# Kernel tuning notes

Measured on AMD Instinct MI355X. Metric: run time of the kernel, lower is better.

The kernel has to match this reference:

```python
import jax, jax.numpy as jnp
import numpy as np

# Regular (dv=3, dc=6) LDPC Tanner graph, rate 1/2
N = 2097152   # variable nodes (code.n)
M = 1048576   # check nodes (H.shape[0])
DV = 3
DC = 6
T = 10        # max_iterations
BC = 4        # c2v bit-width -> 2^(bc-1) = 8 magnitude levels
K = 2 ** (BC - 1)
QUANT_PARAMS = [(2.0, 1.0), (4.0, 1.5), (6.0, 2.0)]


def _make_thresholds():
    """Per-iteration threshold table [T, K]; tau_j = C*(j/(K-1))**gamma."""
    def thr(C, g):
        return [C * (j / (K - 1)) ** g for j in range(K)]
    rows = []
    for t in range(T):
        if t < T // 3:
            C, g = QUANT_PARAMS[0]
        elif t < 2 * T // 3:
            C, g = QUANT_PARAMS[1]
        else:
            C, g = QUANT_PARAMS[-1]
        rows.append(thr(C, g))
    return jnp.asarray(rows, dtype=jnp.float32)


def setup_inputs() -> dict:
    key = jax.random.key(0)
    k_llr, k_beta, k_alpha = jax.random.split(key, 3)
    rng = np.random.default_rng(0)
    # each variable node has exactly DV edges; each check exactly DC edges
    var_idx = np.repeat(np.arange(N, dtype=np.int32), DV)
    chk_idx = rng.permutation(np.repeat(np.arange(M, dtype=np.int32), DC)).astype(np.int32)
    llr = jax.random.normal(k_llr, (N,), dtype=jnp.float32) * 2.0
    # weight init matches nn.Parameter(torch.randn(1)*0.1), one per (iter, degree)
    beta = jax.random.normal(k_beta, (T,), dtype=jnp.float32) * 0.1
    alpha = jax.random.normal(k_alpha, (T,), dtype=jnp.float32) * 0.1
    return {
        "llr": llr,
        "var_idx": jnp.asarray(var_idx),
        "chk_idx": jnp.asarray(chk_idx),
        "beta": beta,
        "alpha": alpha,
        "thresholds": _make_thresholds(),
        "m": M,
    }


def reference(llr, var_idx, chk_idx, beta, alpha, thresholds, m):
    n = llr.shape[0]
    E = var_idx.shape[0]
    eidx = jnp.arange(E, dtype=jnp.int32)
    INF = jnp.float32(jnp.inf)

    def step(v2c, xs):
        b, a, thr = xs  # scalar beta_t, alpha_t, thr [K]
        neg = v2c < 0
        sgn = jnp.where(neg, -1.0, 1.0).astype(v2c.dtype)
        mag = jnp.abs(v2c)
        # --- check node update: min-sum with exclusion (min1/min2) ---
        min1 = jax.ops.segment_min(mag, chk_idx, num_segments=m)
        # first edge attaining the min in each check (ties -> lowest edge id)
        cand = jnp.where(mag <= min1[chk_idx], eidx, E)
        first = jax.ops.segment_min(cand, chk_idx, num_segments=m)
        is_min = eidx == first[chk_idx]
        min2 = jax.ops.segment_min(jnp.where(is_min, INF, mag), chk_idx, num_segments=m)
        min2 = jnp.where(jnp.isinf(min2), min1, min2)  # degree-1 guard
        # sign product excluding self: total parity * own sign
        cnt = jax.ops.segment_sum(neg.astype(jnp.int32), chk_idx, num_segments=m)
        tot = (1 - 2 * (cnt & 1)).astype(v2c.dtype)
        sign_excl = tot[chk_idx] * sgn
        mval = jnp.where(is_min, min2[chk_idx], min1[chk_idx])
        raw = b * sign_excl * mval
        # --- RCQ quantize/dequantize of c2v: snap |raw| down to threshold ---
        q = jnp.clip(jnp.searchsorted(thr, jnp.abs(raw), side="right") - 1, 0, K - 1)
        c2v = jnp.where(raw < 0, -1.0, 1.0) * thr[q]
        # --- variable node update ---
        post = llr + jax.ops.segment_sum(c2v, var_idx, num_segments=n)
        v2c_new = a * (post[var_idx] - c2v)
        return v2c_new, post

    v2c0 = llr[var_idx]
    _, posts = jax.lax.scan(step, v2c0, (beta, alpha, thresholds))
    posterior = posts[-1]
    decoded = (posterior < 0).astype(jnp.int32)
    return decoded, posterior, jnp.int32(beta.shape[0])
```

## Files before the change

### kernel.cpp

```cpp
#include <hip/hip_runtime.h>
#include <stdint.h>

#define NV 2097152
#define MC 1048576
#define EE 6291456
#define TT 10

#define CHUNK 8192
#define NBLK 768
#define FBK 512
#define CPB 2048
#define CSEG 12288
#define FG 512
#define GSEG 12288
#define VBK 256
#define VSEG 24576

__global__ __launch_bounds__(512) void initcur_kernel(uint32_t* __restrict__ gcur) {
    int i = blockIdx.x * 512 + threadIdx.x;
    gcur[i] = (uint32_t)(i & 511) * 12288u;
}

__global__ __launch_bounds__(256) void bin1_kernel(const int* __restrict__ chk_idx,
                                                   uint32_t* __restrict__ gcurA,
                                                   uint32_t* __restrict__ im1_e,
                                                   uint16_t* __restrict__ im1_c) {
    __shared__ uint32_t cnt0[512];
    __shared__ uint32_t aux[512];
    __shared__ uint32_t sA[CHUNK];
    __shared__ uint16_t sB[CHUNK];
    const int tid = threadIdx.x;
    const int rep = tid >> 7;
    const int base = blockIdx.x * CHUNK;
    cnt0[tid] = 0; cnt0[tid + 256] = 0;
    aux[tid] = 0;  aux[tid + 256] = 0;
    __syncthreads();
    int4 cc4[8];
#pragma unroll
    for (int k = 0; k < 8; ++k) cc4[k] = ((const int4*)chk_idx)[(base >> 2) + tid + 256 * k];
    uint32_t br[32];
#pragma unroll
    for (int k = 0; k < 8; ++k) {
        int cv[4] = {cc4[k].x, cc4[k].y, cc4[k].z, cc4[k].w};
#pragma unroll
        for (int ii = 0; ii < 4; ++ii) {
            uint32_t b = (uint32_t)cv[ii] >> 11;
            uint32_t r = atomicAdd(rep ? &aux[b] : &cnt0[b], 1u);
            br[k * 4 + ii] = (b << 13) | r;
        }
    }
    __syncthreads();
    const uint32_t s0 = cnt0[tid] + aux[tid];
    const uint32_t s1 = cnt0[tid + 256] + aux[tid + 256];
    aux[tid] = s0; aux[tid + 256] = s1;
    __syncthreads();
    for (int d = 1; d < 512; d <<= 1) {
        uint32_t a0 = (tid >= d) ? aux[tid - d] : 0u;
        uint32_t a1 = aux[tid + 256 - d];
        __syncthreads();
        aux[tid] += a0; aux[tid + 256] += a1;
        __syncthreads();
    }
    const uint32_t excl0 = aux[tid] - s0;
    const uint32_t excl1 = aux[tid + 256] - s1;
    aux[tid] = excl0; aux[tid + 256] = excl1;
    const uint32_t gb0 = atomicAdd(&gcurA[tid], s0);
    const uint32_t gb1 = atomicAdd(&gcurA[tid + 256], s1);
    __syncthreads();
#pragma unroll
    for (int k = 0; k < 8; ++k) {
        int cv[4] = {cc4[k].x, cc4[k].y, cc4[k].z, cc4[k].w};
#pragma unroll
        for (int ii = 0; ii < 4; ++ii) {
            uint32_t v = br[k * 4 + ii];
            uint32_t b = v >> 13;
            uint32_t r = v & 8191u;
            uint32_t j = aux[b] + (rep ? cnt0[b] : 0u) + r;
            uint32_t e = (uint32_t)(base + (tid + 256 * k) * 4 + ii);
            sA[j] = (b << 23) | e;
            sB[j] = (uint16_t)((uint32_t)cv[ii] & 2047u);
        }
    }
    __syncthreads();
    aux[tid] = gb0 - excl0; aux[tid + 256] = gb1 - excl1;
    __syncthreads();
#pragma unroll 8
    for (int k = 0; k < 32; ++k) {
        int j = tid + 256 * k;
        uint32_t v = sA[j];
        uint32_t b = v >> 23;
        uint32_t addr = aux[b] + (uint32_t)j;
        im1_e[addr] = v & 0x7FFFFFu;
        im1_c[addr] = sB[j];
    }
}

__global__ __launch_bounds__(256) void place1_kernel(const uint32_t* __restrict__ im1_e,
                                                     const uint16_t* __restrict__ im1_c,
                                                     uint32_t* __restrict__ chk_edges,
                                                     uint8_t* __restrict__ b1rank,
                                                     uint32_t* __restrict__ runcntB) {
    __shared__ uint32_t win[CSEG];
    __shared__ uint32_t ccnt[CPB / 2];
    __shared__ uint32_t cntB[VBK];
    const int tid = threadIdx.x, blk = blockIdx.x;
    for (int j = tid; j < CPB / 2; j += 256) ccnt[j] = 0;
    cntB[tid] = 0;
    __syncthreads();
    const size_t cb = (size_t)blk * CSEG;
    for (int k = 0; k < 12; ++k) {
        int j0 = (tid + 256 * k) * 4;
        const uint4 e4 = *(const uint4*)&im1_e[cb + j0];
        const ushort4 c4 = *(const ushort4*)&im1_c[cb + j0];
        uint32_t c, old, s;
        c = c4.x; old = atomicAdd(&ccnt[c >> 1], 1u << ((c & 1) * 16));
        s = (old >> ((c & 1) * 16)) & 0xFFFFu; win[c * 6 + s] = e4.x;
        c = c4.y; old = atomicAdd(&ccnt[c >> 1], 1u << ((c & 1) * 16));
        s = (old >> ((c & 1) * 16)) & 0xFFFFu; win[c * 6 + s] = e4.y;
        c = c4.z; old = atomicAdd(&ccnt[c >> 1], 1u << ((c & 1) * 16));
        s = (old >> ((c & 1) * 16)) & 0xFFFFu; win[c * 6 + s] = e4.z;
        c = c4.w; old = atomicAdd(&ccnt[c >> 1], 1u << ((c & 1) * 16));
        s = (old >> ((c & 1) * 16)) & 0xFFFFu; win[c * 6 + s] = e4.w;
    }
    __syncthreads();
    for (int j = tid; j < CSEG; j += 256) chk_edges[cb + j] = win[j];
    for (int k = 0; k < CSEG / 256; ++k) {
        int lp = tid + 256 * k;
        uint32_t e = win[lp];
        uint32_t bB = (e / 3u) >> 13;
        uint32_t r = atomicAdd(&cntB[bB], 1u);
        b1rank[cb + lp] = (uint8_t)r;
    }
    __syncthreads();
    runcntB[(size_t)tid * FBK + blk] = cntB[tid];
}

__global__ __launch_bounds__(256) void bin2_kernel(const uint32_t* __restrict__ chk_edges,
                                                   uint32_t* __restrict__ gcurB,
                                                   uint32_t* __restrict__ im2_pay,
                                                   uint16_t* __restrict__ im2_el) {
    __shared__ uint32_t cnt0[512];
    __shared__ uint32_t aux[512];
    __shared__ uint32_t sA[CHUNK];
    __shared__ uint16_t sB[CHUNK];
    const int tid = threadIdx.x;
    const int rep = tid >> 7;
    const int base = blockIdx.x * CHUNK;
    cnt0[tid] = 0; cnt0[tid + 256] = 0;
    aux[tid] = 0;  aux[tid + 256] = 0;
    __syncthreads();
    uint4 ee4[8];
#pragma unroll
    for (int k = 0; k < 8; ++k) ee4[k] = ((const uint4*)chk_edges)[(base >> 2) + tid + 256 * k];
    uint32_t br[32];
#pragma unroll
    for (int k = 0; k < 8; ++k) {
        uint32_t ev[4] = {ee4[k].x, ee4[k].y, ee4[k].z, ee4[k].w};
#pragma unroll
        for (int ii = 0; ii < 4; ++ii) {
            uint32_t vb = ev[ii] / 12288u;
            uint32_t r = atomicAdd(rep ? &aux[vb] : &cnt0[vb], 1u);
            br[k * 4 + ii] = (vb << 13) | r;
        }
    }
    __syncthreads();
    const uint32_t s0 = cnt0[tid] + aux[tid];
    const uint32_t s1 = cnt0[tid + 256] + aux[tid + 256];
    aux[tid] = s0; aux[tid + 256] = s1;
    __syncthreads();
    for (int d = 1; d < 512; d <<= 1) {
        uint32_t a0 = (tid >= d) ? aux[tid - d] : 0u;
        uint32_t a1 = aux[tid + 256 - d];
        __syncthreads();
        aux[tid] += a0; aux[tid + 256] += a1;
        __syncthreads();
    }
    const uint32_t excl0 = aux[tid] - s0;
    const uint32_t excl1 = aux[tid + 256] - s1;
    aux[tid] = excl0; aux[tid + 256] = excl1;
    const uint32_t gb0 = atomicAdd(&gcurB[tid], s0);
    const uint32_t gb1 = atomicAdd(&gcurB[tid + 256], s1);
    __syncthreads();
#pragma unroll
    for (int k = 0; k < 8; ++k) {
        uint32_t ev[4] = {ee4[k].x, ee4[k].y, ee4[k].z, ee4[k].w};
#pragma unroll
        for (int ii = 0; ii < 4; ++ii) {
            uint32_t v = br[k * 4 + ii];
            uint32_t vb = v >> 13;
            uint32_t r = v & 8191u;
            uint32_t j = aux[vb] + (rep ? cnt0[vb] : 0u) + r;
            uint32_t pl = (uint32_t)((tid + 256 * k) * 4 + ii);
            sA[j] = (vb << 13) | pl;
            sB[j] = (uint16_t)(ev[ii] - vb * 12288u);
        }
    }
    __syncthreads();
    aux[tid] = gb0 - excl0; aux[tid + 256] = gb1 - excl1;
    __syncthreads();
#pragma unroll 8
    for (int k = 0; k < 32; ++k) {
        int j = tid + 256 * k;
        uint32_t v = sA[j];
        uint32_t vb = v >> 13;
        uint32_t pos = (uint32_t)base + (v & 8191u);
        uint32_t c = pos / 6u;
        uint32_t s = pos - c * 6u;
        uint32_t addr = aux[vb] + (uint32_t)j;
        im2_pay[addr] = (c << 3) | s;
        im2_el[addr] = sB[j];
    }
}

__global__ __launch_bounds__(256) void place2_kernel(const uint32_t* __restrict__ im2_pay,
                                                     const uint16_t* __restrict__ im2_el,
                                                     uint32_t* __restrict__ dest,
                                                     uint8_t* __restrict__ f1rank,
                                                     uint32_t* __restrict__ runcntF) {
    __shared__ uint32_t win2[GSEG];
    __shared__ uint32_t cntF[FBK];
    const int tid = threadIdx.x, g = blockIdx.x;
    cntF[tid] = 0; cntF[tid + 256] = 0;
    __syncthreads();
    const size_t gb = (size_t)g * GSEG;
    for (int k = 0; k < 12; ++k) {
        int j0 = (tid + 256 * k) * 4;
        const uint4 p4 = *(const uint4*)&im2_pay[gb + j0];
        const ushort4 e4 = *(const ushort4*)&im2_el[gb + j0];
        win2[e4.x] = p4.x; win2[e4.y] = p4.y; win2[e4.z] = p4.z; win2[e4.w] = p4.w;
    }
    __syncthreads();
    for (int j = tid; j < GSEG; j += 256) dest[gb + j] = win2[j];
    for (int k = 0; k < GSEG / 256; ++k) {
        int le = tid + 256 * k;
        uint32_t b = (win2[le] >> 3) >> 11;
        uint32_t r = atomicAdd(&cntF[b], 1u);
        f1rank[gb + le] = (uint8_t)r;
    }
    __syncthreads();
    runcntF[(size_t)tid * FG + g] = cntF[tid];
    runcntF[(size_t)(tid + 256) * FG + g] = cntF[tid + 256];
}

__global__ __launch_bounds__(256) void scanF_kernel(const uint32_t* __restrict__ runcntF,
                                                    uint32_t* __restrict__ f1base) {
    __shared__ uint32_t sc[512];
    const int tid = threadIdx.x, b = blockIdx.x;
    uint32_t c0 = runcntF[(size_t)b * FG + tid];
    uint32_t c1 = runcntF[(size_t)b * FG + tid + 256];
    sc[tid] = c0; sc[tid + 256] = c1;
    __syncthreads();
    for (int d = 1; d < 512; d <<= 1) {
        uint32_t a0 = (tid >= d) ? sc[tid - d] : 0u;
        uint32_t a1 = sc[tid + 256 - d];
        __syncthreads();
        sc[tid] += a0; sc[tid + 256] += a1;
        __syncthreads();
    }
    uint32_t base = (uint32_t)b * CSEG;
    f1base[(size_t)tid * FBK + b] = base + sc[tid] - c0;
    f1base[(size_t)(tid + 256) * FBK + b] = base + sc[tid + 256] - c1;
}

__global__ __launch_bounds__(256) void scanB_kernel(const uint32_t* __restrict__ runcntB,
                                                    uint32_t* __restrict__ b1base) {
    __shared__ uint32_t sc[512];
    const int tid = threadIdx.x, bB = blockIdx.x;
    uint32_t c0 = runcntB[(size_t)bB * FBK + tid];
    uint32_t c1 = runcntB[(size_t)bB * FBK + tid + 256];
    sc[tid] = c0; sc[tid + 256] = c1;
    __syncthreads();
    for (int d = 1; d < 512; d <<= 1) {
        uint32_t a0 = (tid >= d) ? sc[tid - d] : 0u;
        uint32_t a1 = sc[tid + 256 - d];
        __syncthreads();
        sc[tid] += a0; sc[tid + 256] += a1;
        __syncthreads();
    }
    uint32_t base = (uint32_t)bB * VSEG;
    b1base[(size_t)tid * VBK + bB] = base + sc[tid] - c0;
    b1base[(size_t)(tid + 256) * VBK + bB] = base + sc[tid + 256] - c1;
}

__global__ __launch_bounds__(256) void fb_kernel(const uint32_t* __restrict__ dest,
                                                 const uint8_t* __restrict__ f1rank,
                                                 const uint32_t* __restrict__ runcntF,
                                                 const uint32_t* __restrict__ f1base,
                                                 uint32_t* __restrict__ goffF,
                                                 uint16_t* __restrict__ f2pos,
                                                 uint16_t* __restrict__ bidxF,
                                                 uint16_t* __restrict__ lvF) {
    __shared__ uint32_t flb[FBK];
    __shared__ uint32_t rowf[FBK];
    __shared__ uint32_t sortv[GSEG];
    const int tid = threadIdx.x, g = blockIdx.x;
    uint32_t c0 = runcntF[(size_t)tid * FG + g];
    uint32_t c1 = runcntF[(size_t)(tid + 256) * FG + g];
    flb[tid] = c0; flb[tid + 256] = c1;
    rowf[tid] = f1base[(size_t)g * FBK + tid];
    rowf[tid + 256] = f1base[(size_t)g * FBK + tid + 256];
    __syncthreads();
    for (int d = 1; d < FBK; d <<= 1) {
        uint32_t a0 = (tid >= d) ? flb[tid - d] : 0u;
        uint32_t a1 = flb[tid + 256 - d];
        __syncthreads();
        flb[tid] += a0; flb[tid + 256] += a1;
        __syncthreads();
    }
    flb[tid] -= c0; flb[tid + 256] -= c1;
    __syncthreads();
    goffF[(size_t)g * FBK + tid] = rowf[tid] - flb[tid];
    goffF[(size_t)g * FBK + tid + 256] = rowf[tid + 256] - flb[tid + 256];
    const size_t gb = (size_t)g * GSEG;
    for (int k = 0; k < GSEG / 256; ++k) {
        int le = tid + 256 * k;
        uint32_t d = dest[gb + le];
        uint32_t r = f1rank[gb + le];
        uint32_t c = d >> 3;
        uint32_t b = c >> 11;
        uint32_t pl = c * 6u + (d & 7u) - b * 12288u;
        sortv[flb[b] + r] = (b << 14) | pl;
    }
    __syncthreads();
    for (int k = 0; k < GSEG / 256; ++k) {
        int j = tid + 256 * k;
        uint32_t v = sortv[j];
        uint32_t b = v >> 14;
        f2pos[rowf[b] - flb[b] + j] = (uint16_t)(v & 16383u);
        bidxF[gb + j] = (uint16_t)b;
    }
    __syncthreads();
    for (int k = 0; k < GSEG / 256; ++k) {
        int le = tid + 256 * k;
        uint32_t d = dest[gb + le];
        uint32_t r = f1rank[gb + le];
        uint32_t b = (d >> 3) >> 11;
        sortv[flb[b] + r] = (uint32_t)(le / 3);
    }
    __syncthreads();
    for (int k = 0; k < GSEG / 256; ++k) {
        int j = tid + 256 * k;
        lvF[gb + j] = (uint16_t)sortv[j];
    }
}

__global__ __launch_bounds__(256) void bb_kernel(const uint32_t* __restrict__ chk_edges,
                                                 const uint8_t* __restrict__ b1rank,
                                                 const uint32_t* __restrict__ runcntB,
                                                 const uint32_t* __restrict__ b1base,
                                                 uint32_t* __restrict__ goffB,
                                                 uint16_t* __restrict__ b2pos,
                                                 uint8_t* __restrict__ bidxB,
                                                 uint16_t* __restrict__ lposB) {
    __shared__ uint32_t blb[VBK];
    __shared__ uint32_t rowb[VBK];
    __shared__ uint32_t sortv[CSEG];
    const int tid = threadIdx.x, blk = blockIdx.x;
    uint32_t c0 = runcntB[(size_t)tid * FBK + blk];
    blb[tid] = c0;
    rowb[tid] = b1base[(size_t)blk * VBK + tid];
    __syncthreads();
    for (int d = 1; d < VBK; d <<= 1) {
        uint32_t a0 = (tid >= d) ? blb[tid - d] : 0u;
        __syncthreads();
        blb[tid] += a0;
        __syncthreads();
    }
    blb[tid] -= c0;
    __syncthreads();
    goffB[(size_t)blk * VBK + tid] = rowb[tid] - blb[tid];
    const size_t cb = (size_t)blk * CSEG;
    for (int k = 0; k < CSEG / 256; ++k) {
        int lp = tid + 256 * k;
        uint32_t e = chk_edges[cb + lp];
        uint32_t r = b1rank[cb + lp];
        uint32_t bB = (e / 3u) >> 13;
        uint32_t elocal = e - bB * VSEG;
        sortv[blb[bB] + r] = (bB << 15) | elocal;
    }
    __syncthreads();
    for (int k = 0; k < CSEG / 256; ++k) {
        int j = tid + 256 * k;
        uint32_t v = sortv[j];
        uint32_t bB = v >> 15;
        b2pos[rowb[bB] - blb[bB] + j] = (uint16_t)(v & 32767u);
        bidxB[cb + j] = (uint8_t)bB;
    }
    __syncthreads();
    for (int k = 0; k < CSEG / 256; ++k) {
        int lp = tid + 256 * k;
        uint32_t e = chk_edges[cb + lp];
        uint32_t r = b1rank[cb + lp];
        uint32_t bB = (e / 3u) >> 13;
        sortv[blb[bB] + r] = (uint32_t)lp;
    }
    __syncthreads();
    for (int k = 0; k < CSEG / 256; ++k) {
        int j = tid + 256 * k;
        lposB[cb + j] = (uint16_t)sortv[j];
    }
}

__global__ __launch_bounds__(256) void check_kernel(const float* __restrict__ finterm,
                                                    const uint16_t* __restrict__ f2pos,
                                                    uint32_t* __restrict__ einfo,
                                                    const uint16_t* __restrict__ lposB,
                                                    const uint8_t* __restrict__ bidxB,
                                                    const uint32_t* __restrict__ goffB,
                                                    uint8_t* __restrict__ binterm,
                                                    const float* __restrict__ beta,
                                                    const float* __restrict__ alpha,
                                                    const float* __restrict__ thresholds,
                                                    int t) {
    __shared__ __align__(16) float fwin[CSEG];
    __shared__ uint32_t grow[VBK];
    __shared__ float tp[8];
    uint32_t* ewin = (uint32_t*)fwin;
    const int tid = threadIdx.x, blk = blockIdx.x;
    if (tid < 8) tp[tid] = thresholds[((t > 0) ? (t - 1) : 0) * 8 + tid];
    grow[tid] = goffB[(size_t)blk * VBK + tid];
    const size_t cb = (size_t)blk * CSEG;
    for (int k = 0; k < 12; ++k) {
        int j0 = (tid + 256 * k) * 4;
        const float4 f4 = *(const float4*)&finterm[cb + j0];
        const ushort4 p4 = *(const ushort4*)&f2pos[cb + j0];
        fwin[p4.x] = f4.x; fwin[p4.y] = f4.y; fwin[p4.z] = f4.z; fwin[p4.w] = f4.w;
    }
    __syncthreads();

    const float aPrev = (t > 0) ? alpha[t - 1] : 1.0f;
    const float b = beta[t];
    const float* thc = thresholds + t * 8;
    const float th1 = thc[1], th2 = thc[2], th3 = thc[3], th4 = thc[4];
    const float th5 = thc[5], th6 = thc[6], th7 = thc[7];
    const uint32_t signb = (b < 0.0f) ? 1u : 0u;

    uint32_t wreg[8];
    for (int i = 0; i < 8; ++i) {
        int lc = tid + 256 * i;
        uint32_t wprev = (t > 0) ? einfo[blk * CPB + lc] : 0u;
        float mags[6];
        uint32_t sgn[6];
        uint32_t parity = 0;
        uint64_t minkey = ~0ull;
#pragma unroll
        for (int j = 0; j < 6; ++j) {
            float p = fwin[lc * 6 + j];
            uint32_t nib = (wprev >> (4 * j)) & 15u;
            float mg0 = tp[nib & 7u];
            float c2v = (nib & 8u) ? -mg0 : mg0;
            float x = aPrev * (p - c2v);
            uint32_t s = (x < 0.0f) ? 1u : 0u;
            parity ^= s;
            sgn[j] = s;
            float mg = fabsf(x);
            mags[j] = mg;
            uint64_t key = (((uint64_t)__float_as_uint(mg)) << 3) | (uint32_t)j;
            minkey = (key < minkey) ? key : minkey;
        }
        float min1 = __uint_as_float((uint32_t)(minkey >> 3));
        uint32_t fs = (uint32_t)(minkey & 7u);
        float min2 = INFINITY;
#pragma unroll
        for (int j = 0; j < 6; ++j) {
            if ((uint32_t)j != fs) min2 = fminf(min2, mags[j]);
        }
        float m1 = fabsf(b * min1);
        float m2 = fabsf(b * min2);
        uint32_t q1 = (uint32_t)(m1 >= th1) + (uint32_t)(m1 >= th2) + (uint32_t)(m1 >= th3)
                    + (uint32_t)(m1 >= th4) + (uint32_t)(m1 >= th5) + (uint32_t)(m1 >= th6)
                    + (uint32_t)(m1 >= th7);
        uint32_t q2 = (uint32_t)(m2 >= th1) + (uint32_t)(m2 >= th2) + (uint32_t)(m2 >= th3)
                    + (uint32_t)(m2 >= th4) + (uint32_t)(m2 >= th5) + (uint32_t)(m2 >= th6)
                    + (uint32_t)(m2 >= th7);
        uint32_t w = 0;
#pragma unroll
        for (int j = 0; j < 6; ++j) {
            uint32_t neg = signb ^ parity ^ sgn[j];
            uint32_t q = ((uint32_t)j == fs) ? q2 : q1;
            w |= ((neg << 3) | q) << (4 * j);
        }
        wreg[i] = w;
    }
    __syncthreads();
    for (int i = 0; i < 8; ++i) {
        int lc = tid + 256 * i;
        ewin[lc] = wreg[i];
        einfo[blk * CPB + lc] = wreg[i];
    }
    __syncthreads();
    for (int k = 0; k < 12; ++k) {
        int j0 = (tid + 256 * k) * 4;
        const ushort4 lp4 = *(const ushort4*)&lposB[cb + j0];
        const uchar4 b4 = *(const uchar4*)&bidxB[cb + j0];
        uint32_t lp, word;
        lp = lp4.x; word = ewin[lp / 6u];
        binterm[grow[b4.x] + j0 + 0] = (uint8_t)((word >> ((lp - 6u * (lp / 6u)) * 4u)) & 15u);
        lp = lp4.y; word = ewin[lp / 6u];
        binterm[grow[b4.y] + j0 + 1] = (uint8_t)((word >> ((lp - 6u * (lp / 6u)) * 4u)) & 15u);
        lp = lp4.z; word = ewin[lp / 6u];
        binterm[grow[b4.z] + j0 + 2] = (uint8_t)((word >> ((lp - 6u * (lp / 6u)) * 4u)) & 15u);
        lp = lp4.w; word = ewin[lp / 6u];
        binterm[grow[b4.w] + j0 + 3] = (uint8_t)((word >> ((lp - 6u * (lp / 6u)) * 4u)) & 15u);
    }
}

__global__ __launch_bounds__(512) void var_kernel(const float* __restrict__ llr,
                                                  const uint8_t* __restrict__ binterm,
                                                  const uint16_t* __restrict__ b2pos,
                                                  const uint16_t* __restrict__ lvF,
                                                  const uint16_t* __restrict__ bidxF,
                                                  const uint32_t* __restrict__ goffF,
                                                  float* __restrict__ finterm,
                                                  const float* __restrict__ thresholds,
                                                  int t, int mode,
                                                  float* __restrict__ out) {
    __shared__ uint8_t nwin[VSEG];
    __shared__ float pwin[4096];
    __shared__ uint32_t growF[FBK];
    __shared__ float tl[8];
    const int tid = threadIdx.x, vblk = blockIdx.x;
    if (tid < 8) tl[tid] = thresholds[t * 8 + tid];
    if (mode != 1) {
        const size_t vb = (size_t)vblk * VSEG;
        for (int k = 0; k < 12; ++k) {
            int i0 = (tid + 512 * k) * 4;
            const uchar4 n4 = *(const uchar4*)&binterm[vb + i0];
            const ushort4 p4 = *(const ushort4*)&b2pos[vb + i0];
            nwin[p4.x] = n4.x; nwin[p4.y] = n4.y; nwin[p4.z] = n4.z; nwin[p4.w] = n4.w;
        }
    }
    __syncthreads();
    for (int h = 0; h < 2; ++h) {
        if (h == 1) __syncthreads();
        for (int i = 0; i < 8; ++i) {
            int lv = tid + 512 * i;
            int lvfull = h * 4096 + lv;
            int v = vblk * 8192 + lvfull;
            float post;
            if (mode == 1) {
                post = llr[v];
            } else {
                uint32_t n0 = nwin[3 * lvfull], n1 = nwin[3 * lvfull + 1], n2 = nwin[3 * lvfull + 2];
                float c0 = (n0 & 8u) ? -tl[n0 & 7u] : tl[n0 & 7u];
                float c1 = (n1 & 8u) ? -tl[n1 & 7u] : tl[n1 & 7u];
                float c2 = (n2 & 8u) ? -tl[n2 & 7u] : tl[n2 & 7u];
                post = llr[v] + ((c0 + c1) + c2);
            }
            pwin[lv] = post;
            if (mode == 2) {
                out[v] = (post < 0.0f) ? 1.0f : 0.0f;
                out[NV + v] = post;
                if (v == 0) out[2 * NV] = 10.0f;
            }
        }
        if (mode == 2) continue;
        const int g = 2 * vblk + h;
        growF[tid] = goffF[(size_t)g * FBK + tid];
        __syncthreads();
        const size_t gb = (size_t)g * GSEG;
        for (int k = 0; k < 6; ++k) {
            int j0 = (tid + 512 * k) * 4;
            const ushort4 lv4 = *(const ushort4*)&lvF[gb + j0];
            const ushort4 b4 = *(const ushort4*)&bidxF[gb + j0];
            finterm[growF[b4.x] + j0 + 0] = pwin[lv4.x];
            finterm[growF[b4.y] + j0 + 1] = pwin[lv4.y];
            finterm[growF[b4.z] + j0 + 2] = pwin[lv4.z];
            finterm[growF[b4.w] + j0 + 3] = pwin[lv4.w];
        }
    }
}

extern "C" void kernel_launch(void* const* d_in, const int* in_sizes, int n_in,
                              void* d_out, int out_size, void* d_ws, size_t ws_size,
                              hipStream_t stream) {
    const float* llr        = (const float*)d_in[0];
    const int*   var_idx    = (const int*)d_in[1];   (void)var_idx;
    const int*   chk_idx    = (const int*)d_in[2];
    const float* beta       = (const float*)d_in[3];
    const float* alpha      = (const float*)d_in[4];
    const float* thresholds = (const float*)d_in[5];
    float* out = (float*)d_out;

    char* wsb = (char*)d_ws;
    float*    finterm   = (float*)(wsb + 0);
    uint16_t* f2pos     = (uint16_t*)(wsb + 25165824);
    uint16_t* lvF       = (uint16_t*)(wsb + 37748736);
    uint16_t* bidxF     = (uint16_t*)(wsb + 50331648);
    uint16_t* lposB     = (uint16_t*)(wsb + 62914560);
    uint16_t* b2pos     = (uint16_t*)(wsb + 75497472);
    uint8_t*  bidxB     = (uint8_t*)(wsb + 88080384);
    uint8_t*  binterm   = (uint8_t*)(wsb + 94371840);
    uint32_t* einfo     = (uint32_t*)(wsb + 100663296);
    uint32_t* chk_edges = (uint32_t*)(wsb + 104857600);
    uint32_t* dest      = (uint32_t*)(wsb + 130023424);
    uint32_t* im1_e     = (uint32_t*)(wsb + 155189248);
    uint16_t* im1_c     = (uint16_t*)(wsb + 180355072);
    uint32_t* im2_pay   = im1_e;
    uint16_t* im2_el    = im1_c;
    uint8_t*  f1rank    = (uint8_t*)(wsb + 192937984);
    uint8_t*  b1rank    = (uint8_t*)(wsb + 199229440);
    uint32_t* runcntF   = (uint32_t*)(wsb + 205520896);
    uint32_t* f1base    = (uint32_t*)(wsb + 206569472);
    uint32_t* runcntB   = (uint32_t*)(wsb + 207618048);
    uint32_t* b1base    = (uint32_t*)(wsb + 208142336);
    uint32_t* goffF     = (uint32_t*)(wsb + 208666624);
    uint32_t* goffB     = (uint32_t*)(wsb + 209715200);
    uint32_t* gcur      = (uint32_t*)(wsb + 210239488);
    uint32_t* gcurA     = gcur;
    uint32_t* gcurB     = gcur + 512;

    const int B = 256;
    initcur_kernel<<<2, 512, 0, stream>>>(gcur);
    bin1_kernel<<<NBLK, B, 0, stream>>>(chk_idx, gcurA, im1_e, im1_c);
    place1_kernel<<<FBK, B, 0, stream>>>(im1_e, im1_c, chk_edges, b1rank, runcntB);
    bin2_kernel<<<NBLK, B, 0, stream>>>(chk_edges, gcurB, im2_pay, im2_el);
    place2_kernel<<<FG, B, 0, stream>>>(im2_pay, im2_el, dest, f1rank, runcntF);
    scanF_kernel<<<FBK, B, 0, stream>>>(runcntF, f1base);
    fb_kernel<<<FG, B, 0, stream>>>(dest, f1rank, runcntF, f1base, goffF, f2pos, bidxF, lvF);
    scanB_kernel<<<VBK, B, 0, stream>>>(runcntB, b1base);
    bb_kernel<<<FBK, B, 0, stream>>>(chk_edges, b1rank, runcntB, b1base, goffB, b2pos, bidxB, lposB);
    var_kernel<<<VBK, 512, 0, stream>>>(llr, binterm, b2pos, lvF, bidxF, goffF,
                                        finterm, thresholds, 0, 1, out);

    for (int t = 0; t < TT; ++t) {
        check_kernel<<<FBK, B, 0, stream>>>(finterm, f2pos, einfo, lposB, bidxB, goffB,
                                            binterm, beta, alpha, thresholds, t);
        var_kernel<<<VBK, 512, 0, stream>>>(llr, binterm, b2pos, lvF, bidxF, goffF,
                                            finterm, thresholds, t,
                                            (t == TT - 1) ? 2 : 0, out);
    }
}
```

Measured before the change: 742.1 us.

## Gather packed check messages directly in var kernel, drop backward scatter path

Measured after the change: 866.9 us. +16.8%, slower.

```diff
diff --git a/kernel.cpp b/kernel.cpp
--- a/kernel.cpp
+++ b/kernel.cpp
@@ -14,7 +14,6 @@
 #define FG 512
 #define GSEG 12288
 #define VBK 256
-#define VSEG 24576
 
 __global__ __launch_bounds__(512) void initcur_kernel(uint32_t* __restrict__ gcur) {
     int i = blockIdx.x * 512 + threadIdx.x;
@@ -97,15 +96,11 @@
 
 __global__ __launch_bounds__(256) void place1_kernel(const uint32_t* __restrict__ im1_e,
                                                      const uint16_t* __restrict__ im1_c,
-                                                     uint32_t* __restrict__ chk_edges,
-                                                     uint8_t* __restrict__ b1rank,
-                                                     uint32_t* __restrict__ runcntB) {
+                                                     uint32_t* __restrict__ chk_edges) {
     __shared__ uint32_t win[CSEG];
     __shared__ uint32_t ccnt[CPB / 2];
-    __shared__ uint32_t cntB[VBK];
     const int tid = threadIdx.x, blk = blockIdx.x;
     for (int j = tid; j < CPB / 2; j += 256) ccnt[j] = 0;
-    cntB[tid] = 0;
     __syncthreads();
     const size_t cb = (size_t)blk * CSEG;
     for (int k = 0; k < 12; ++k) {
@@ -124,15 +119,6 @@
     }
     __syncthreads();
     for (int j = tid; j < CSEG; j += 256) chk_edges[cb + j] = win[j];
-    for (int k = 0; k < CSEG / 256; ++k) {
-        int lp = tid + 256 * k;
-        uint32_t e = win[lp];
-        uint32_t bB = (e / 3u) >> 13;
-        uint32_t r = atomicAdd(&cntB[bB], 1u);
-        b1rank[cb + lp] = (uint8_t)r;
-    }
-    __syncthreads();
-    runcntB[(size_t)tid * FBK + blk] = cntB[tid];
 }
 
 __global__ __launch_bounds__(256) void bin2_kernel(const uint32_t* __restrict__ chk_edges,
@@ -260,26 +246,6 @@
     uint32_t base = (uint32_t)b * CSEG;
     f1base[(size_t)tid * FBK + b] = base + sc[tid] - c0;
     f1base[(size_t)(tid + 256) * FBK + b] = base + sc[tid + 256] - c1;
-}
-
-__global__ __launch_bounds__(256) void scanB_kernel(const uint32_t* __restrict__ runcntB,
-                                                    uint32_t* __restrict__ b1base) {
-    __shared__ uint32_t sc[512];
-    const int tid = threadIdx.x, bB = blockIdx.x;
-    uint32_t c0 = runcntB[(size_t)bB * FBK + tid];
-    uint32_t c1 = runcntB[(size_t)bB * FBK + tid + 256];
-    sc[tid] = c0; sc[tid + 256] = c1;
-    __syncthreads();
-    for (int d = 1; d < 512; d <<= 1) {
-        uint32_t a0 = (tid >= d) ? sc[tid - d] : 0u;
-        uint32_t a1 = sc[tid + 256 - d];
-        __syncthreads();
-        sc[tid] += a0; sc[tid + 256] += a1;
-        __syncthreads();
-    }
-    uint32_t base = (uint32_t)bB * VSEG;
-    b1base[(size_t)tid * VBK + bB] = base + sc[tid] - c0;
-    b1base[(size_t)(tid + 256) * VBK + bB] = base + sc[tid + 256] - c1;
 }
 
 __global__ __launch_bounds__(256) void fb_kernel(const uint32_t* __restrict__ dest,
@@ -344,81 +310,17 @@
     }
 }
 
-__global__ __launch_bounds__(256) void bb_kernel(const uint32_t* __restrict__ chk_edges,
-                                                 const uint8_t* __restrict__ b1rank,
-                                                 const uint32_t* __restrict__ runcntB,
-                                                 const uint32_t* __restrict__ b1base,
-                                                 uint32_t* __restrict__ goffB,
-                                                 uint16_t* __restrict__ b2pos,
-                                                 uint8_t* __restrict__ bidxB,
-                                                 uint16_t* __restrict__ lposB) {
-    __shared__ uint32_t blb[VBK];
-    __shared__ uint32_t rowb[VBK];
-    __shared__ uint32_t sortv[CSEG];
-    const int tid = threadIdx.x, blk = blockIdx.x;
-    uint32_t c0 = runcntB[(size_t)tid * FBK + blk];
-    blb[tid] = c0;
-    rowb[tid] = b1base[(size_t)blk * VBK + tid];
-    __syncthreads();
-    for (int d = 1; d < VBK; d <<= 1) {
-        uint32_t a0 = (tid >= d) ? blb[tid - d] : 0u;
-        __syncthreads();
-        blb[tid] += a0;
-        __syncthreads();
-    }
-    blb[tid] -= c0;
-    __syncthreads();
-    goffB[(size_t)blk * VBK + tid] = rowb[tid] - blb[tid];
-    const size_t cb = (size_t)blk * CSEG;
-    for (int k = 0; k < CSEG / 256; ++k) {
-        int lp = tid + 256 * k;
-        uint32_t e = chk_edges[cb + lp];
-        uint32_t r = b1rank[cb + lp];
-        uint32_t bB = (e / 3u) >> 13;
-        uint32_t elocal = e - bB * VSEG;
-        sortv[blb[bB] + r] = (bB << 15) | elocal;
-    }
-    __syncthreads();
-    for (int k = 0; k < CSEG / 256; ++k) {
-        int j = tid + 256 * k;
-        uint32_t v = sortv[j];
-        uint32_t bB = v >> 15;
-        b2pos[rowb[bB] - blb[bB] + j] = (uint16_t)(v & 32767u);
-        bidxB[cb + j] = (uint8_t)bB;
-    }
-    __syncthreads();
-    for (int k = 0; k < CSEG / 256; ++k) {
-        int lp = tid + 256 * k;
-        uint32_t e = chk_edges[cb + lp];
-        uint32_t r = b1rank[cb + lp];
-        uint32_t bB = (e / 3u) >> 13;
-        sortv[blb[bB] + r] = (uint32_t)lp;
-    }
-    __syncthreads();
-    for (int k = 0; k < CSEG / 256; ++k) {
-        int j = tid + 256 * k;
-        lposB[cb + j] = (uint16_t)sortv[j];
-    }
-}
-
 __global__ __launch_bounds__(256) void check_kernel(const float* __restrict__ finterm,
                                                     const uint16_t* __restrict__ f2pos,
                                                     uint32_t* __restrict__ einfo,
-                                                    const uint16_t* __restrict__ lposB,
-                                                    const uint8_t* __restrict__ bidxB,
-                                                    const uint32_t* __restrict__ goffB,
-                                                    uint8_t* __restrict__ binterm,
                                                     const float* __restrict__ beta,
                                                     const float* __restrict__ alpha,
                                                     const float* __restrict__ thresholds,
                                                     int t) {
     __shared__ __align__(16) float fwin[CSEG];
-    __shared__ uint32_t grow[VBK];
     __shared__ float tp[8];
-    uint32_t* ewin = (uint32_t*)fwin;
     const int tid = threadIdx.x, blk = blockIdx.x;
     if (tid < 8) tp[tid] = thresholds[((t > 0) ? (t - 1) : 0) * 8 + tid];
-    grow[tid] = goffB[(size_t)blk * VBK + tid];
     const size_t cb = (size_t)blk * CSEG;
     for (int k = 0; k < 12; ++k) {
         int j0 = (tid + 256 * k) * 4;
@@ -435,7 +337,6 @@
     const float th5 = thc[5], th6 = thc[6], th7 = thc[7];
     const uint32_t signb = (b < 0.0f) ? 1u : 0u;
 
-    uint32_t wreg[8];
     for (int i = 0; i < 8; ++i) {
         int lc = tid + 256 * i;
         uint32_t wprev = (t > 0) ? einfo[blk * CPB + lc] : 0u;
@@ -480,34 +381,13 @@
             uint32_t q = ((uint32_t)j == fs) ? q2 : q1;
             w |= ((neg << 3) | q) << (4 * j);
         }
-        wreg[i] = w;
-    }
-    __syncthreads();
-    for (int i = 0; i < 8; ++i) {
-        int lc = tid + 256 * i;
-        ewin[lc] = wreg[i];
-        einfo[blk * CPB + lc] = wreg[i];
-    }
-    __syncthreads();
-    for (int k = 0; k < 12; ++k) {
-        int j0 = (tid + 256 * k) * 4;
-        const ushort4 lp4 = *(const ushort4*)&lposB[cb + j0];
-        const uchar4 b4 = *(const uchar4*)&bidxB[cb + j0];
-        uint32_t lp, word;
-        lp = lp4.x; word = ewin[lp / 6u];
-        binterm[grow[b4.x] + j0 + 0] = (uint8_t)((word >> ((lp - 6u * (lp / 6u)) * 4u)) & 15u);
-        lp = lp4.y; word = ewin[lp / 6u];
-        binterm[grow[b4.y] + j0 + 1] = (uint8_t)((word >> ((lp - 6u * (lp / 6u)) * 4u)) & 15u);
-        lp = lp4.z; word = ewin[lp / 6u];
-        binterm[grow[b4.z] + j0 + 2] = (uint8_t)((word >> ((lp - 6u * (lp / 6u)) * 4u)) & 15u);
-        lp = lp4.w; word = ewin[lp / 6u];
-        binterm[grow[b4.w] + j0 + 3] = (uint8_t)((word >> ((lp - 6u * (lp / 6u)) * 4u)) & 15u);
+        einfo[blk * CPB + lc] = w;
     }
 }
 
 __global__ __launch_bounds__(512) void var_kernel(const float* __restrict__ llr,
-                                                  const uint8_t* __restrict__ binterm,
-                                                  const uint16_t* __restrict__ b2pos,
+                                                  const uint32_t* __restrict__ dest,
+                                                  const uint32_t* __restrict__ einfo,
                                                   const uint16_t* __restrict__ lvF,
                                                   const uint16_t* __restrict__ bidxF,
                                                   const uint32_t* __restrict__ goffF,
@@ -515,46 +395,40 @@
                                                   const float* __restrict__ thresholds,
                                                   int t, int mode,
                                                   float* __restrict__ out) {
-    __shared__ uint8_t nwin[VSEG];
-    __shared__ float pwin[4096];
+    __shared__ float pwin[8192];
     __shared__ uint32_t growF[FBK];
     __shared__ float tl[8];
     const int tid = threadIdx.x, vblk = blockIdx.x;
     if (tid < 8) tl[tid] = thresholds[t * 8 + tid];
-    if (mode != 1) {
-        const size_t vb = (size_t)vblk * VSEG;
-        for (int k = 0; k < 12; ++k) {
-            int i0 = (tid + 512 * k) * 4;
-            const uchar4 n4 = *(const uchar4*)&binterm[vb + i0];
-            const ushort4 p4 = *(const ushort4*)&b2pos[vb + i0];
-            nwin[p4.x] = n4.x; nwin[p4.y] = n4.y; nwin[p4.z] = n4.z; nwin[p4.w] = n4.w;
-        }
-    }
-    __syncthreads();
+    __syncthreads();
+    for (int i = 0; i < 16; ++i) {
+        int lv = tid + 512 * i;
+        int v = vblk * 8192 + lv;
+        float post;
+        if (mode == 1) {
+            post = llr[v];
+        } else {
+            const size_t e0 = 3 * (size_t)v;
+            uint32_t d0 = dest[e0], d1 = dest[e0 + 1], d2 = dest[e0 + 2];
+            uint32_t w0 = einfo[d0 >> 3], w1 = einfo[d1 >> 3], w2 = einfo[d2 >> 3];
+            uint32_t n0 = (w0 >> ((d0 & 7u) * 4u)) & 15u;
+            uint32_t n1 = (w1 >> ((d1 & 7u) * 4u)) & 15u;
+            uint32_t n2 = (w2 >> ((d2 & 7u) * 4u)) & 15u;
+            float c0 = (n0 & 8u) ? -tl[n0 & 7u] : tl[n0 & 7u];
+            float c1 = (n1 & 8u) ? -tl[n1 & 7u] : tl[n1 & 7u];
+            float c2 = (n2 & 8u) ? -tl[n2 & 7u] : tl[n2 & 7u];
+            post = llr[v] + ((c0 + c1) + c2);
+        }
+        pwin[lv] = post;
+        if (mode == 2) {
+            out[v] = (post < 0.0f) ? 1.0f : 0.0f;
+            out[NV + v] = post;
+            if (v == 0) out[2 * NV] = 10.0f;
+        }
+    }
+    __syncthreads();
+    if (mode == 2) return;
     for (int h = 0; h < 2; ++h) {
-        if (h == 1) __syncthreads();
-        for (int i = 0; i < 8; ++i) {
-            int lv = tid + 512 * i;
-            int lvfull = h * 4096 + lv;
-            int v = vblk * 8192 + lvfull;
-            float post;
-            if (mode == 1) {
-                post = llr[v];
-            } else {
-                uint32_t n0 = nwin[3 * lvfull], n1 = nwin[3 * lvfull + 1], n2 = nwin[3 * lvfull + 2];
-                float c0 = (n0 & 8u) ? -tl[n0 & 7u] : tl[n0 & 7u];
-                float c1 = (n1 & 8u) ? -tl[n1 & 7u] : tl[n1 & 7u];
-                float c2 = (n2 & 8u) ? -tl[n2 & 7u] : tl[n2 & 7u];
-                post = llr[v] + ((c0 + c1) + c2);
-            }
-            pwin[lv] = post;
-            if (mode == 2) {
-                out[v] = (post < 0.0f) ? 1.0f : 0.0f;
-                out[NV + v] = post;
-                if (v == 0) out[2 * NV] = 10.0f;
-            }
-        }
-        if (mode == 2) continue;
         const int g = 2 * vblk + h;
         growF[tid] = goffF[(size_t)g * FBK + tid];
         __syncthreads();
@@ -563,11 +437,12 @@
             int j0 = (tid + 512 * k) * 4;
             const ushort4 lv4 = *(const ushort4*)&lvF[gb + j0];
             const ushort4 b4 = *(const ushort4*)&bidxF[gb + j0];
-            finterm[growF[b4.x] + j0 + 0] = pwin[lv4.x];
-            finterm[growF[b4.y] + j0 + 1] = pwin[lv4.y];
-            finterm[growF[b4.z] + j0 + 2] = pwin[lv4.z];
-            finterm[growF[b4.w] + j0 + 3] = pwin[lv4.w];
-        }
+            finterm[growF[b4.x] + j0 + 0] = pwin[h * 4096 + lv4.x];
+            finterm[growF[b4.y] + j0 + 1] = pwin[h * 4096 + lv4.y];
+            finterm[growF[b4.z] + j0 + 2] = pwin[h * 4096 + lv4.z];
+            finterm[growF[b4.w] + j0 + 3] = pwin[h * 4096 + lv4.w];
+        }
+        __syncthreads();
     }
 }
 
@@ -587,10 +462,6 @@
     uint16_t* f2pos     = (uint16_t*)(wsb + 25165824);
     uint16_t* lvF       = (uint16_t*)(wsb + 37748736);
     uint16_t* bidxF     = (uint16_t*)(wsb + 50331648);
-    uint16_t* lposB     = (uint16_t*)(wsb + 62914560);
-    uint16_t* b2pos     = (uint16_t*)(wsb + 75497472);
-    uint8_t*  bidxB     = (uint8_t*)(wsb + 88080384);
-    uint8_t*  binterm   = (uint8_t*)(wsb + 94371840);
     uint32_t* einfo     = (uint32_t*)(wsb + 100663296);
     uint32_t* chk_edges = (uint32_t*)(wsb + 104857600);
     uint32_t* dest      = (uint32_t*)(wsb + 130023424);
@@ -599,13 +470,9 @@
     uint32_t* im2_pay   = im1_e;
     uint16_t* im2_el    = im1_c;
     uint8_t*  f1rank    = (uint8_t*)(wsb + 192937984);
-    uint8_t*  b1rank    = (uint8_t*)(wsb + 199229440);
     uint32_t* runcntF   = (uint32_t*)(wsb + 205520896);
     uint32_t* f1base    = (uint32_t*)(wsb + 206569472);
-    uint32_t* runcntB   = (uint32_t*)(wsb + 207618048);
-    uint32_t* b1base    = (uint32_t*)(wsb + 208142336);
     uint32_t* goffF     = (uint32_t*)(wsb + 208666624);
-    uint32_t* goffB     = (uint32_t*)(wsb + 209715200);
     uint32_t* gcur      = (uint32_t*)(wsb + 210239488);
     uint32_t* gcurA     = gcur;
     uint32_t* gcurB     = gcur + 512;
@@ -613,20 +480,17 @@
     const int B = 256;
     initcur_kernel<<<2, 512, 0, stream>>>(gcur);
     bin1_kernel<<<NBLK, B, 0, stream>>>(chk_idx, gcurA, im1_e, im1_c);
-    place1_kernel<<<FBK, B, 0, stream>>>(im1_e, im1_c, chk_edges, b1rank, runcntB);
+    place1_kernel<<<FBK, B, 0, stream>>>(im1_e, im1_c, chk_edges);
     bin2_kernel<<<NBLK, B, 0, stream>>>(chk_edges, gcurB, im2_pay, im2_el);
     place2_kernel<<<FG, B, 0, stream>>>(im2_pay, im2_el, dest, f1rank, runcntF);
     scanF_kernel<<<FBK, B, 0, stream>>>(runcntF, f1base);
     fb_kernel<<<FG, B, 0, stream>>>(dest, f1rank, runcntF, f1base, goffF, f2pos, bidxF, lvF);
-    scanB_kernel<<<VBK, B, 0, stream>>>(runcntB, b1base);
-    bb_kernel<<<FBK, B, 0, stream>>>(chk_edges, b1rank, runcntB, b1base, goffB, b2pos, bidxB, lposB);
-    var_kernel<<<VBK, 512, 0, stream>>>(llr, binterm, b2pos, lvF, bidxF, goffF,
+    var_kernel<<<VBK, 512, 0, stream>>>(llr, dest, einfo, lvF, bidxF, goffF,
                                         finterm, thresholds, 0, 1, out);
 
     for (int t = 0; t < TT; ++t) {
-        check_kernel<<<FBK, B, 0, stream>>>(finterm, f2pos, einfo, lposB, bidxB, goffB,
-                                            binterm, beta, alpha, thresholds, t);
-        var_kernel<<<VBK, 512, 0, stream>>>(llr, binterm, b2pos, lvF, bidxF, goffF,
+        check_kernel<<<FBK, B, 0, stream>>>(finterm, f2pos, einfo, beta, alpha, thresholds, t);
+        var_kernel<<<VBK, 512, 0, stream>>>(llr, dest, einfo, lvF, bidxF, goffF,
                                             finterm, thresholds, t,
                                             (t == TT - 1) ? 2 : 0, out);
     }
```
